# Performance work log

Hardware: AMD Instinct MI355X
Metric: run time of the kernel (lower is better)

## Reference

```python
import jax, jax.numpy as jnp
import numpy as np

C = 256      # channels (multiple of 32 for GroupNorm)
K = 3        # kernel
PAD = 1      # padding
G = 32       # GroupNorm groups
EPS = 1e-5


def setup_inputs() -> dict:
    key = jax.random.key(0)
    ks = jax.random.split(key, 7)
    B, H, W = 4, 64, 64
    return {
        "x": jax.random.normal(ks[0], (B, C, H, W), jnp.float32),
        "offset": jax.random.normal(ks[1], (B, 2 * K * K, H, W), jnp.float32),
        "weight": jax.random.normal(ks[2], (C, C, K, K), jnp.float32) * 0.01,
        "att_w": jax.random.normal(ks[3], (1, C), jnp.float32) * 0.01,
        "att_b": jnp.zeros((1,), jnp.float32),
        "gamma": jnp.ones((C,), jnp.float32),
        "beta": jnp.zeros((C,), jnp.float32),
    }


def _bilinear_one(xb, py, px):
    # xb: [C, H, W]; py, px: [KK, H, W] fractional sample coords (zero-pad outside)
    H, W = xb.shape[1], xb.shape[2]
    y0 = jnp.floor(py)
    x0 = jnp.floor(px)
    y1 = y0 + 1.0
    x1 = x0 + 1.0
    wy1 = py - y0
    wy0 = 1.0 - wy1
    wx1 = px - x0
    wx0 = 1.0 - wx1

    def g(yi, xi):
        valid = (yi >= 0) & (yi < H) & (xi >= 0) & (xi < W)
        yc = jnp.clip(yi, 0, H - 1).astype(jnp.int32)
        xc = jnp.clip(xi, 0, W - 1).astype(jnp.int32)
        return xb[:, yc, xc] * valid[None].astype(xb.dtype)  # [C, KK, H, W]

    return (g(y0, x0) * (wy0 * wx0)[None] + g(y0, x1) * (wy0 * wx1)[None]
            + g(y1, x0) * (wy1 * wx0)[None] + g(y1, x1) * (wy1 * wx1)[None])


def reference(x, offset, weight, att_w, att_b, gamma, beta):
    B, Cc, H, W = x.shape
    KK = K * K
    off = offset.reshape(B, KK, 2, H, W)  # (dy, dx) per kernel tap
    ii, jj = jnp.meshgrid(jnp.arange(K), jnp.arange(K), indexing='ij')
    dky = (ii - PAD).reshape(KK).astype(x.dtype)
    dkx = (jj - PAD).reshape(KK).astype(x.dtype)
    ys = jnp.arange(H, dtype=x.dtype)
    xs = jnp.arange(W, dtype=x.dtype)
    # sample coords [B, KK, H, W]
    py = ys[None, :, None] + dky[:, None, None] + off[:, :, 0]
    px = xs[None, None, :] + dkx[:, None, None] + off[:, :, 1]

    # deformable unfold: [B, C, KK, H, W]
    xu = jax.vmap(_bilinear_one)(x, py, px)

    # max over kernel taps -> channel attention gate
    xm = xu.max(axis=2)  # [B, C, H, W]
    att = jax.nn.sigmoid(jnp.einsum('bchw,oc->bohw', xm, att_w)
                         + att_b[None, :, None, None])  # [B, 1, H, W]

    # gate the unfolded samples, then emulate the conv as one GEMM
    xw = xu * att[:, :, None]  # broadcast over C, KK
    cols = xw.transpose(1, 2, 0, 3, 4).reshape(Cc * KK, B * H * W)  # [C*KK, BHW]
    out = (weight.reshape(Cc, Cc * KK) @ cols).reshape(Cc, B, H, W).transpose(1, 0, 2, 3)

    # GroupNorm(32, C) + ReLU
    og = out.reshape(B, G, Cc // G, H, W)
    mu = og.mean(axis=(2, 3, 4), keepdims=True)
    var = og.var(axis=(2, 3, 4), keepdims=True)
    on = ((og - mu) * jax.lax.rsqrt(var + EPS)).reshape(B, Cc, H, W)
    return jax.nn.relu(on * gamma[None, :, None, None] + beta[None, :, None, None])
```

## Files before the change

### kernel.cpp

```cpp
#include <hip/hip_runtime.h>

#define CT 256
#define KDIM 2304
#define COLP 296

typedef unsigned short u16;
typedef _Float16 h2 __attribute__((ext_vector_type(2)));
typedef _Float16 h8 __attribute__((ext_vector_type(8)));
typedef __attribute__((ext_vector_type(4))) float f32x4;

__device__ __forceinline__ unsigned pkh(float a, float b) {
    h2 r; r[0] = (_Float16)a; r[1] = (_Float16)b;
    return __builtin_bit_cast(unsigned, r);
}

__device__ __forceinline__ void gload_lds16(const uint4* g, u16* l) {
    __builtin_amdgcn_global_load_lds((const __attribute__((address_space(1))) void*)g,
                                     (__attribute__((address_space(3))) void*)l, 16, 0, 0);
}

__global__ __launch_bounds__(256) void k_prep(const float* __restrict__ x, uint4* __restrict__ xi,
                                              const float* __restrict__ wgt, uint4* __restrict__ pw)
{
    if (blockIdx.x < 2048) {
        int u = blockIdx.x * 256 + threadIdx.x;
        int bcg = u >> 12, p = u & 4095;
        const float* xp = x + (((size_t)bcg) << 15) + p;
        unsigned r[4];
#pragma unroll
        for (int i = 0; i < 4; ++i)
            r[i] = pkh(xp[(size_t)(2 * i) << 12], xp[(size_t)(2 * i + 1) << 12]);
        uint4 o; o.x = r[0]; o.y = r[1]; o.z = r[2]; o.w = r[3];
        xi[u] = o;
    } else {
        int u = (blockIdx.x - 2048) * 256 + threadIdx.x;
        int kc = u >> 10, rm = u & 1023;
        int m = rm >> 2, j = rm & 3;
        int round = kc / 9, tap = kc - round * 9;
        const float* src = wgt + (size_t)m * KDIM + tap;
        int c0 = round * 32 + j * 8;
        unsigned q[4];
#pragma unroll
        for (int i = 0; i < 4; ++i)
            q[i] = pkh(src[(size_t)(c0 + 2 * i) * 9], src[(size_t)(c0 + 2 * i + 1) * 9]);
        uint4 o; o.x = q[0]; o.y = q[1]; o.z = q[2]; o.w = q[3];
        pw[u] = o;
    }
}

__device__ __forceinline__ void gather_one(int it2, int sp, int xsb, size_t gfall,
                                           const uint2* s_wt, const int2* s_off,
                                           const u16* Xs, u16* col,
                                           const uint4* __restrict__ xi, int rbase, int nw)
{
    int tap = it2 >> 5, nn = it2 & 31;
    uint2 wp = s_wt[it2];
    h2 w01 = __builtin_bit_cast(h2, wp.x);
    h2 w23 = __builtin_bit_cast(h2, wp.y);
    h2 wxp = (h2){w01[0], w01[0]}, wyp = (h2){w01[1], w01[1]};
    h2 wzp = (h2){w23[0], w23[0]}, wwp = (h2){w23[1], w23[1]};
    int2 of = s_off[it2];
    int P00 = of.x & 0xffff, P01 = (of.x >> 16) & 0xffff;
    int P10 = of.y & 0xffff, P11 = (of.y >> 16) & 0xffff;
    uint4 c00, c01, c10, c11;
    int Q;
    Q = P00 - rbase;
    if ((unsigned)Q < (unsigned)nw) c00 = *(const uint4*)&Xs[xsb + Q * 8]; else c00 = xi[gfall + P00];
    Q = P01 - rbase;
    if ((unsigned)Q < (unsigned)nw) c01 = *(const uint4*)&Xs[xsb + Q * 8]; else c01 = xi[gfall + P01];
    Q = P10 - rbase;
    if ((unsigned)Q < (unsigned)nw) c10 = *(const uint4*)&Xs[xsb + Q * 8]; else c10 = xi[gfall + P10];
    Q = P11 - rbase;
    if ((unsigned)Q < (unsigned)nw) c11 = *(const uint4*)&Xs[xsb + Q * 8]; else c11 = xi[gfall + P11];
    const unsigned* a00 = (const unsigned*)&c00;
    const unsigned* a01 = (const unsigned*)&c01;
    const unsigned* a10 = (const unsigned*)&c10;
    const unsigned* a11 = (const unsigned*)&c11;
    unsigned o[4];
#pragma unroll
    for (int q = 0; q < 4; ++q) {
        h2 r = wxp * __builtin_bit_cast(h2, a00[q]) + wyp * __builtin_bit_cast(h2, a01[q])
             + wzp * __builtin_bit_cast(h2, a10[q]) + wwp * __builtin_bit_cast(h2, a11[q]);
        o[q] = __builtin_bit_cast(unsigned, r);
    }
    uint4 ov; ov.x = o[0]; ov.y = o[1]; ov.z = o[2]; ov.w = o[3];
    *(uint4*)&col[nn * COLP + tap * 32 + sp * 8] = ov;
}

__global__ __launch_bounds__(512, 2) void k_main(const uint4* __restrict__ xi, const float* __restrict__ off,
                                                 const uint4* __restrict__ pw, const float* __restrict__ att_w,
                                                 const float* __restrict__ att_b,
                                                 float* __restrict__ outp, float* __restrict__ gnpart)
{
    __shared__ uint2 s_wt[288];
    __shared__ int2 s_off[288];
    __shared__ u16 Xs[4 * 6656];
    __shared__ u16 col[32 * COLP];
    __shared__ float s_att[32];

    int rowblk = blockIdx.x >> 1, half = blockIdx.x & 1;
    int b = rowblk >> 6, h = rowblk & 63, n0 = half * 32;
    int tid = threadIdx.x;
    int lane = tid & 63, w = tid >> 6;
    int l15 = lane & 15, kb = lane >> 4;
    int wm = w * 32;
    int nn_a = w * 4 + (lane >> 4);
    int ca = (lane & 15) * 2;

    for (int e = tid; e < 288; e += 512) {
        int kk = e >> 5, wl = e & 31;
        int ww_ = n0 + wl;
        int ky = kk / 3, kx = kk - ky * 3;
        float dy = off[((size_t)(b * 18 + 2 * kk) * 64 + h) * 64 + ww_];
        float dx = off[((size_t)(b * 18 + 2 * kk + 1) * 64 + h) * 64 + ww_];
        float py = (float)(h + ky - 1) + dy;
        float px = (float)(ww_ + kx - 1) + dx;
        float y0f = floorf(py), x0f = floorf(px);
        int y0 = (int)y0f, x0 = (int)x0f;
        float fy = py - y0f, fx = px - x0f;
        float vy0 = (y0 >= 0 && y0 < 64) ? 1.f : 0.f;
        float vy1 = (y0 >= -1 && y0 < 63) ? 1.f : 0.f;
        float vx0 = (x0 >= 0 && x0 < 64) ? 1.f : 0.f;
        float vx1 = (x0 >= -1 && x0 < 63) ? 1.f : 0.f;
        float w0 = (1.f - fy) * (1.f - fx) * vy0 * vx0;
        float w1 = (1.f - fy) * fx * vy0 * vx1;
        float w2 = fy * (1.f - fx) * vy1 * vx0;
        float w3 = fy * fx * vy1 * vx1;
        uint2 wp;
        wp.x = pkh(w0, w1);
        wp.y = pkh(w2, w3);
        int yc0 = min(max(y0, 0), 63), yc1 = min(max(y0 + 1, 0), 63);
        int xc0 = min(max(x0, 0), 63), xc1 = min(max(x0 + 1, 0), 63);
        s_wt[e] = wp;
        s_off[e] = make_int2((yc0 * 64 + xc0) | ((yc0 * 64 + xc1) << 16),
                             (yc1 * 64 + xc0) | ((yc1 * 64 + xc1) << 16));
    }

    int r0 = max(0, h - 6), r1 = min(63, h + 6);
    int nrows = r1 - r0 + 1, nw = nrows * 64, rbase = r0 * 64;
    size_t xib = (size_t)(b * 32) << 12;

    float att_acc = 0.f;
    f32x4 acc[2][2];
#pragma unroll
    for (int mt = 0; mt < 2; ++mt)
#pragma unroll
        for (int nt = 0; nt < 2; ++nt) acc[mt][nt] = (f32x4){0.f, 0.f, 0.f, 0.f};

    int pwoff[2];
#pragma unroll
    for (int mt = 0; mt < 2; ++mt) pwoff[mt] = (wm + mt * 16 + l15) * 4 + kb;

#pragma unroll
    for (int cgl = 0; cgl < 2; ++cgl)
        for (int e = tid; e < nw; e += 512)
            gload_lds16(&xi[xib + ((size_t)cgl << 12) + rbase + e], &Xs[(cgl * 6656 + e * 8)]);

    for (int stage = 0; stage < 16; ++stage) {
        int buf = stage & 1;
        int s2 = stage & 1;
        __syncthreads();
        if (stage < 15) {
            size_t nb = xib + ((size_t)((stage + 1) * 2) << 12) + rbase;
#pragma unroll
            for (int cgl = 0; cgl < 2; ++cgl)
                for (int e = tid; e < nw; e += 512)
                    gload_lds16(&xi[nb + ((size_t)cgl << 12) + e],
                                &Xs[(((buf ^ 1) * 2 + cgl) * 6656 + e * 8)]);
        }
        {
            int it = tid;
            int cgl = (it >= 288) ? 1 : 0;
            gather_one(it - cgl * 288, s2 * 2 + cgl, (buf * 2 + cgl) * 6656,
                       xib + ((size_t)(stage * 2 + cgl) << 12), s_wt, s_off, Xs, col, xi, rbase, nw);
            if (tid >= 448) {
                int it2 = tid + 64;
                gather_one(it2 - 288, s2 * 2 + 1, (buf * 2 + 1) * 6656,
                           xib + ((size_t)(stage * 2 + 1) << 12), s_wt, s_off, Xs, col, xi, rbase, nw);
            }
        }

        if (stage & 1) {
            int round = stage >> 1;
            __syncthreads();

            uint4 aa[4][2];
#pragma unroll
            for (int ts = 0; ts < 4; ++ts)
#pragma unroll
                for (int mt = 0; mt < 2; ++mt)
                    aa[ts][mt] = pw[(size_t)(round * 9 + ts) * 1024 + pwoff[mt]];

            {
                int sp = ca >> 3, co = ca & 7;
                const u16* base = &col[nn_a * COLP + sp * 8 + co];
                float m0 = -1e30f, m1 = -1e30f;
#pragma unroll
                for (int t = 0; t < 9; ++t) {
                    unsigned v = *(const unsigned*)(base + t * 32);
                    h2 vv = __builtin_bit_cast(h2, v);
                    m0 = fmaxf(m0, (float)vv[0]);
                    m1 = fmaxf(m1, (float)vv[1]);
                }
                int cb = round * 32 + ca;
                att_acc += att_w[cb] * m0 + att_w[cb + 1] * m1;
            }

#pragma unroll
            for (int ts = 0; ts < 9; ++ts) {
                h8 bf[2];
#pragma unroll
                for (int nt = 0; nt < 2; ++nt)
                    bf[nt] = *(const h8*)&col[(nt * 16 + l15) * COLP + ts * 32 + kb * 8];
                h8 af[2];
#pragma unroll
                for (int mt = 0; mt < 2; ++mt) af[mt] = __builtin_bit_cast(h8, aa[ts & 3][mt]);
                if (ts + 4 < 9) {
#pragma unroll
                    for (int mt = 0; mt < 2; ++mt)
                        aa[ts & 3][mt] = pw[(size_t)(round * 9 + ts + 4) * 1024 + pwoff[mt]];
                }
#pragma unroll
                for (int mt = 0; mt < 2; ++mt)
#pragma unroll
                    for (int nt = 0; nt < 2; ++nt)
                        acc[mt][nt] = __builtin_amdgcn_mfma_f32_16x16x32_f16(af[mt], bf[nt], acc[mt][nt], 0, 0, 0);
            }
        }
    }

#pragma unroll
    for (int d = 1; d <= 8; d <<= 1) att_acc += __shfl_xor(att_acc, d);
    if ((lane & 15) == 0) s_att[nn_a] = 1.f / (1.f + expf(-(att_acc + att_b[0])));
    __syncthreads();

    float attn[2];
#pragma unroll
    for (int nt = 0; nt < 2; ++nt) attn[nt] = s_att[nt * 16 + l15];

#pragma unroll
    for (int mt = 0; mt < 2; ++mt) {
        float s1 = 0.f, s2 = 0.f;
#pragma unroll
        for (int nt = 0; nt < 2; ++nt)
#pragma unroll
            for (int r = 0; r < 4; ++r) {
                float v = acc[mt][nt][r] * attn[nt];
                int m = wm + mt * 16 + kb * 4 + r;
                outp[(((size_t)(b * CT + m)) << 12) + h * 64 + n0 + nt * 16 + l15] = v;
                s1 += v; s2 += v * v;
            }
#pragma unroll
        for (int d = 1; d <= 16; d <<= 1) {
            s1 += __shfl_xor(s1, d);
            s2 += __shfl_xor(s2, d);
        }
        if ((lane & 31) == 0) {
            int gidx = w * 4 + mt * 2 + (kb >> 1);
            gnpart[blockIdx.x * 64 + gidx * 2] = s1;
            gnpart[blockIdx.x * 64 + gidx * 2 + 1] = s2;
        }
    }
}

__global__ __launch_bounds__(256) void k_gn(const float* __restrict__ gnpart, const float* __restrict__ gamma,
                                            const float* __restrict__ beta, float* __restrict__ outp)
{
    __shared__ float rs1[128], rs2[128];
    __shared__ float s_stat[2];
    int bg = blockIdx.x;
    int b = bg >> 5, g = bg & 31;
    int tid = threadIdx.x;
    if (tid < 128) {
        int blk = (b * 64 + (tid >> 1)) * 2 + (tid & 1);
        rs1[tid] = gnpart[blk * 64 + g * 2];
        rs2[tid] = gnpart[blk * 64 + g * 2 + 1];
    }
    __syncthreads();
    if (tid < 64) {
        float a = rs1[tid] + rs1[tid + 64];
        float c = rs2[tid] + rs2[tid + 64];
#pragma unroll
        for (int d = 1; d <= 32; d <<= 1) {
            a += __shfl_xor(a, d);
            c += __shfl_xor(c, d);
        }
        if (tid == 0) {
            float mean = a * (1.f / 32768.f);
            float var = c * (1.f / 32768.f) - mean * mean;
            s_stat[0] = mean;
            s_stat[1] = rsqrtf(var + 1e-5f);
        }
    }
    __syncthreads();
    float mean = s_stat[0], rstd = s_stat[1];
    float4* p4 = (float4*)(outp + ((size_t)(b * CT + g * 8) << 12));
    for (int i = tid; i < 8192; i += 256) {
        int c = g * 8 + (i >> 10);
        float ga = gamma[c], be = beta[c];
        float4 v = p4[i];
        float4 r;
        r.x = fmaxf((v.x - mean) * rstd * ga + be, 0.f);
        r.y = fmaxf((v.y - mean) * rstd * ga + be, 0.f);
        r.z = fmaxf((v.z - mean) * rstd * ga + be, 0.f);
        r.w = fmaxf((v.w - mean) * rstd * ga + be, 0.f);
        p4[i] = r;
    }
}

extern "C" void kernel_launch(void* const* d_in, const int* in_sizes, int n_in,
                              void* d_out, int out_size, void* d_ws, size_t ws_size,
                              hipStream_t stream)
{
    const float* x = (const float*)d_in[0];
    const float* off = (const float*)d_in[1];
    const float* wgt = (const float*)d_in[2];
    const float* attw = (const float*)d_in[3];
    const float* attb = (const float*)d_in[4];
    const float* gamma = (const float*)d_in[5];
    const float* beta = (const float*)d_in[6];
    float* outp = (float*)d_out;

    char* ws = (char*)d_ws;
    uint4* xi = (uint4*)ws;
    uint4* pw = (uint4*)(ws + 8388608);
    float* gnpart = (float*)(ws + 9568256);

    k_prep<<<dim3(2336), dim3(256), 0, stream>>>(x, xi, wgt, pw);
    k_main<<<dim3(512), dim3(512), 0, stream>>>(xi, off, pw, attw, attb, outp, gnpart);
    k_gn<<<dim3(128), dim3(256), 0, stream>>>(gnpart, gamma, beta, outp);
}
```

Baseline: 147.1 us.

## Gather directly from global into double-buffered col, overlapping with MFMA

```diff
diff --git a/kernel.cpp b/kernel.cpp
--- a/kernel.cpp
+++ b/kernel.cpp
@@ -3,6 +3,7 @@
 #define CT 256
 #define KDIM 2304
 #define COLP 296
+#define CSZ (32 * COLP)
 
 typedef unsigned short u16;
 typedef _Float16 h2 __attribute__((ext_vector_type(2)));
@@ -12,11 +13,6 @@
 __device__ __forceinline__ unsigned pkh(float a, float b) {
     h2 r; r[0] = (_Float16)a; r[1] = (_Float16)b;
     return __builtin_bit_cast(unsigned, r);
-}
-
-__device__ __forceinline__ void gload_lds16(const uint4* g, u16* l) {
-    __builtin_amdgcn_global_load_lds((const __attribute__((address_space(1))) void*)g,
-                                     (__attribute__((address_space(3))) void*)l, 16, 0, 0);
 }
 
 __global__ __launch_bounds__(256) void k_prep(const float* __restrict__ x, uint4* __restrict__ xi,
@@ -48,54 +44,58 @@
     }
 }
 
-__device__ __forceinline__ void gather_one(int it2, int sp, int xsb, size_t gfall,
-                                           const uint2* s_wt, const int2* s_off,
-                                           const u16* Xs, u16* col,
-                                           const uint4* __restrict__ xi, int rbase, int nw)
-{
-    int tap = it2 >> 5, nn = it2 & 31;
-    uint2 wp = s_wt[it2];
-    h2 w01 = __builtin_bit_cast(h2, wp.x);
-    h2 w23 = __builtin_bit_cast(h2, wp.y);
+struct GB {
+    uint4 c00, c01, c10, c11;
+    unsigned wx, wy;
+    int dst;
+};
+
+__device__ __forceinline__ void g_load(int it, int round, size_t xib,
+                                       const uint2* s_wt, const int2* s_off,
+                                       const uint4* __restrict__ xi, GB& g)
+{
+    int sp = it / 288;
+    int rem = it - sp * 288;
+    uint2 wp = s_wt[rem];
+    int2 of = s_off[rem];
+    g.wx = wp.x; g.wy = wp.y;
+    const uint4* gp = xi + xib + ((size_t)((round << 2) + sp) << 12);
+    g.c00 = gp[of.x & 0xffff];
+    g.c01 = gp[(of.x >> 16) & 0xffff];
+    g.c10 = gp[of.y & 0xffff];
+    g.c11 = gp[(of.y >> 16) & 0xffff];
+    g.dst = (rem & 31) * COLP + (rem >> 5) * 32 + (sp << 3);
+}
+
+__device__ __forceinline__ void g_fin(const GB& g, u16* colb)
+{
+    h2 w01 = __builtin_bit_cast(h2, g.wx);
+    h2 w23 = __builtin_bit_cast(h2, g.wy);
     h2 wxp = (h2){w01[0], w01[0]}, wyp = (h2){w01[1], w01[1]};
     h2 wzp = (h2){w23[0], w23[0]}, wwp = (h2){w23[1], w23[1]};
-    int2 of = s_off[it2];
-    int P00 = of.x & 0xffff, P01 = (of.x >> 16) & 0xffff;
-    int P10 = of.y & 0xffff, P11 = (of.y >> 16) & 0xffff;
-    uint4 c00, c01, c10, c11;
-    int Q;
-    Q = P00 - rbase;
-    if ((unsigned)Q < (unsigned)nw) c00 = *(const uint4*)&Xs[xsb + Q * 8]; else c00 = xi[gfall + P00];
-    Q = P01 - rbase;
-    if ((unsigned)Q < (unsigned)nw) c01 = *(const uint4*)&Xs[xsb + Q * 8]; else c01 = xi[gfall + P01];
-    Q = P10 - rbase;
-    if ((unsigned)Q < (unsigned)nw) c10 = *(const uint4*)&Xs[xsb + Q * 8]; else c10 = xi[gfall + P10];
-    Q = P11 - rbase;
-    if ((unsigned)Q < (unsigned)nw) c11 = *(const uint4*)&Xs[xsb + Q * 8]; else c11 = xi[gfall + P11];
-    const unsigned* a00 = (const unsigned*)&c00;
-    const unsigned* a01 = (const unsigned*)&c01;
-    const unsigned* a10 = (const unsigned*)&c10;
-    const unsigned* a11 = (const unsigned*)&c11;
+    const unsigned* a00 = (const unsigned*)&g.c00;
+    const unsigned* a01 = (const unsigned*)&g.c01;
+    const unsigned* a10 = (const unsigned*)&g.c10;
+    const unsigned* a11 = (const unsigned*)&g.c11;
     unsigned o[4];
 #pragma unroll
     for (int q = 0; q < 4; ++q) {
-        h2 r = wxp * __builtin_bit_cast(h2, a00[q]) + wyp * __builtin_bit_cast(h2, a01[q])
-             + wzp * __builtin_bit_cast(h2, a10[q]) + wwp * __builtin_bit_cast(h2, a11[q]);
-        o[q] = __builtin_bit_cast(unsigned, r);
+        h2 rr = wxp * __builtin_bit_cast(h2, a00[q]) + wyp * __builtin_bit_cast(h2, a01[q])
+              + wzp * __builtin_bit_cast(h2, a10[q]) + wwp * __builtin_bit_cast(h2, a11[q]);
+        o[q] = __builtin_bit_cast(unsigned, rr);
     }
     uint4 ov; ov.x = o[0]; ov.y = o[1]; ov.z = o[2]; ov.w = o[3];
-    *(uint4*)&col[nn * COLP + tap * 32 + sp * 8] = ov;
-}
-
-__global__ __launch_bounds__(512, 2) void k_main(const uint4* __restrict__ xi, const float* __restrict__ off,
+    *(uint4*)&colb[g.dst] = ov;
+}
+
+__global__ __launch_bounds__(512, 4) void k_main(const uint4* __restrict__ xi, const float* __restrict__ off,
                                                  const uint4* __restrict__ pw, const float* __restrict__ att_w,
                                                  const float* __restrict__ att_b,
                                                  float* __restrict__ outp, float* __restrict__ gnpart)
 {
     __shared__ uint2 s_wt[288];
     __shared__ int2 s_off[288];
-    __shared__ u16 Xs[4 * 6656];
-    __shared__ u16 col[32 * COLP];
+    __shared__ u16 col[2 * CSZ];
     __shared__ float s_att[32];
 
     int rowblk = blockIdx.x >> 1, half = blockIdx.x & 1;
@@ -136,8 +136,6 @@
                              (yc1 * 64 + xc0) | ((yc1 * 64 + xc1) << 16));
     }
 
-    int r0 = max(0, h - 6), r1 = min(63, h + 6);
-    int nrows = r1 - r0 + 1, nw = nrows * 64, rbase = r0 * 64;
     size_t xib = (size_t)(b * 32) << 12;
 
     float att_acc = 0.f;
@@ -151,82 +149,87 @@
 #pragma unroll
     for (int mt = 0; mt < 2; ++mt) pwoff[mt] = (wm + mt * 16 + l15) * 4 + kb;
 
-#pragma unroll
-    for (int cgl = 0; cgl < 2; ++cgl)
-        for (int e = tid; e < nw; e += 512)
-            gload_lds16(&xi[xib + ((size_t)cgl << 12) + rbase + e], &Xs[(cgl * 6656 + e * 8)]);
-
-    for (int stage = 0; stage < 16; ++stage) {
-        int buf = stage & 1;
-        int s2 = stage & 1;
+    __syncthreads();
+
+    {
+        GB g0, g1;
+        g_load(tid, 0, xib, s_wt, s_off, xi, g0);
+        g_load(tid + 512, 0, xib, s_wt, s_off, xi, g1);
+        g_fin(g0, col);
+        g_fin(g1, col);
+        if (tid < 128) {
+            GB g2;
+            g_load(tid + 1024, 0, xib, s_wt, s_off, xi, g2);
+            g_fin(g2, col);
+        }
+    }
+
+    uint4 aa[4][2];
+#pragma unroll
+    for (int ts = 0; ts < 4; ++ts)
+#pragma unroll
+        for (int mt = 0; mt < 2; ++mt)
+            aa[ts][mt] = pw[(size_t)ts * 1024 + pwoff[mt]];
+
+    __syncthreads();
+
+    for (int r = 0; r < 8; ++r) {
+        u16* cb = col + (r & 1) * CSZ;
+        u16* nb = col + ((r & 1) ^ 1) * CSZ;
+
+        GB g0, g1, g2;
+        if (r < 7) g_load(tid, r + 1, xib, s_wt, s_off, xi, g0);
+
+        {
+            int spa = ca >> 3, co = ca & 7;
+            const u16* base = &cb[nn_a * COLP + spa * 8 + co];
+            float m0 = -1e30f, m1 = -1e30f;
+#pragma unroll
+            for (int t = 0; t < 9; ++t) {
+                unsigned v = *(const unsigned*)(base + t * 32);
+                h2 vv = __builtin_bit_cast(h2, v);
+                m0 = fmaxf(m0, (float)vv[0]);
+                m1 = fmaxf(m1, (float)vv[1]);
+            }
+            int cbx = r * 32 + ca;
+            att_acc += att_w[cbx] * m0 + att_w[cbx + 1] * m1;
+        }
+
+#pragma unroll
+        for (int ts = 0; ts < 9; ++ts) {
+            h8 bf[2];
+#pragma unroll
+            for (int nt = 0; nt < 2; ++nt)
+                bf[nt] = *(const h8*)&cb[(nt * 16 + l15) * COLP + ts * 32 + kb * 8];
+            h8 af[2];
+#pragma unroll
+            for (int mt = 0; mt < 2; ++mt) af[mt] = __builtin_bit_cast(h8, aa[ts & 3][mt]);
+            if (ts + 4 < 9) {
+#pragma unroll
+                for (int mt = 0; mt < 2; ++mt)
+                    aa[ts & 3][mt] = pw[(size_t)(r * 9 + ts + 4) * 1024 + pwoff[mt]];
+            } else if (r < 7) {
+                int tsp = (ts == 8) ? 0 : (ts - 4);
+#pragma unroll
+                for (int mt = 0; mt < 2; ++mt)
+                    aa[tsp][mt] = pw[(size_t)((r + 1) * 9 + tsp) * 1024 + pwoff[mt]];
+            }
+#pragma unroll
+            for (int mt = 0; mt < 2; ++mt)
+#pragma unroll
+                for (int nt = 0; nt < 2; ++nt)
+                    acc[mt][nt] = __builtin_amdgcn_mfma_f32_16x16x32_f16(af[mt], bf[nt], acc[mt][nt], 0, 0, 0);
+            if (ts == 2 && r < 7) {
+                g_fin(g0, nb);
+                g_load(tid + 512, r + 1, xib, s_wt, s_off, xi, g1);
+            }
+            if (ts == 5 && r < 7) {
+                g_fin(g1, nb);
+                if (tid < 128) g_load(tid + 1024, r + 1, xib, s_wt, s_off, xi, g2);
+            }
+        }
+        if (r < 7 && tid < 128) g_fin(g2, nb);
         __syncthreads();
-        if (stage < 15) {
-            size_t nb = xib + ((size_t)((stage + 1) * 2) << 12) + rbase;
-#pragma unroll
-            for (int cgl = 0; cgl < 2; ++cgl)
-                for (int e = tid; e < nw; e += 512)
-                    gload_lds16(&xi[nb + ((size_t)cgl << 12) + e],
-                                &Xs[(((buf ^ 1) * 2 + cgl) * 6656 + e * 8)]);
-        }
-        {
-            int it = tid;
-            int cgl = (it >= 288) ? 1 : 0;
-            gather_one(it - cgl * 288, s2 * 2 + cgl, (buf * 2 + cgl) * 6656,
-                       xib + ((size_t)(stage * 2 + cgl) << 12), s_wt, s_off, Xs, col, xi, rbase, nw);
-            if (tid >= 448) {
-                int it2 = tid + 64;
-                gather_one(it2 - 288, s2 * 2 + 1, (buf * 2 + 1) * 6656,
-                           xib + ((size_t)(stage * 2 + 1) << 12), s_wt, s_off, Xs, col, xi, rbase, nw);
-            }
-        }
-
-        if (stage & 1) {
-            int round = stage >> 1;
-            __syncthreads();
-
-            uint4 aa[4][2];
-#pragma unroll
-            for (int ts = 0; ts < 4; ++ts)
-#pragma unroll
-                for (int mt = 0; mt < 2; ++mt)
-                    aa[ts][mt] = pw[(size_t)(round * 9 + ts) * 1024 + pwoff[mt]];
-
-            {
-                int sp = ca >> 3, co = ca & 7;
-                const u16* base = &col[nn_a * COLP + sp * 8 + co];
-                float m0 = -1e30f, m1 = -1e30f;
-#pragma unroll
-                for (int t = 0; t < 9; ++t) {
-                    unsigned v = *(const unsigned*)(base + t * 32);
-                    h2 vv = __builtin_bit_cast(h2, v);
-                    m0 = fmaxf(m0, (float)vv[0]);
-                    m1 = fmaxf(m1, (float)vv[1]);
-                }
-                int cb = round * 32 + ca;
-                att_acc += att_w[cb] * m0 + att_w[cb + 1] * m1;
-            }
-
-#pragma unroll
-            for (int ts = 0; ts < 9; ++ts) {
-                h8 bf[2];
-#pragma unroll
-                for (int nt = 0; nt < 2; ++nt)
-                    bf[nt] = *(const h8*)&col[(nt * 16 + l15) * COLP + ts * 32 + kb * 8];
-                h8 af[2];
-#pragma unroll
-                for (int mt = 0; mt < 2; ++mt) af[mt] = __builtin_bit_cast(h8, aa[ts & 3][mt]);
-                if (ts + 4 < 9) {
-#pragma unroll
-                    for (int mt = 0; mt < 2; ++mt)
-                        aa[ts & 3][mt] = pw[(size_t)(round * 9 + ts + 4) * 1024 + pwoff[mt]];
-                }
-#pragma unroll
-                for (int mt = 0; mt < 2; ++mt)
-#pragma unroll
-                    for (int nt = 0; nt < 2; ++nt)
-                        acc[mt][nt] = __builtin_amdgcn_mfma_f32_16x16x32_f16(af[mt], bf[nt], acc[mt][nt], 0, 0, 0);
-            }
-        }
     }
 
 #pragma unroll
```

After: 168.7 us. 14.7% more time.

## Double-buffer im2col tile to overlap gather with MFMA, remap blocks per XCD

Applied to the files above, without the earlier changes.

```diff
diff --git a/kernel.cpp b/kernel.cpp
--- a/kernel.cpp
+++ b/kernel.cpp
@@ -3,6 +3,8 @@
 #define CT 256
 #define KDIM 2304
 #define COLP 296
+#define CCOL (32 * COLP)
+#define XSP 4608
 
 typedef unsigned short u16;
 typedef _Float16 h2 __attribute__((ext_vector_type(2)));
@@ -94,12 +96,18 @@
 {
     __shared__ uint2 s_wt[288];
     __shared__ int2 s_off[288];
-    __shared__ u16 Xs[4 * 6656];
-    __shared__ u16 col[32 * COLP];
+    __shared__ u16 Xs[4 * XSP];
+    __shared__ u16 col[2 * CCOL];
     __shared__ float s_att[32];
 
-    int rowblk = blockIdx.x >> 1, half = blockIdx.x & 1;
-    int b = rowblk >> 6, h = rowblk & 63, n0 = half * 32;
+    int bid = blockIdx.x;
+    int xcd = bid & 7, idx = bid >> 3;
+    int b = xcd >> 1;
+    int local = ((xcd & 1) << 6) + idx;
+    int h = local >> 1, half = local & 1;
+    int lbid = b * 128 + local;
+    int n0 = half * 32;
+
     int tid = threadIdx.x;
     int lane = tid & 63, w = tid >> 6;
     int l15 = lane & 15, kb = lane >> 4;
@@ -136,8 +144,8 @@
                              (yc1 * 64 + xc0) | ((yc1 * 64 + xc1) << 16));
     }
 
-    int r0 = max(0, h - 6), r1 = min(63, h + 6);
-    int nrows = r1 - r0 + 1, nw = nrows * 64, rbase = r0 * 64;
+    int r0c = max(0, h - 4), r1c = min(63, h + 4);
+    int nrows = r1c - r0c + 1, nw = nrows * 64, rbase = r0c * 64;
     size_t xib = (size_t)(b * 32) << 12;
 
     float att_acc = 0.f;
@@ -154,11 +162,10 @@
 #pragma unroll
     for (int cgl = 0; cgl < 2; ++cgl)
         for (int e = tid; e < nw; e += 512)
-            gload_lds16(&xi[xib + ((size_t)cgl << 12) + rbase + e], &Xs[(cgl * 6656 + e * 8)]);
+            gload_lds16(&xi[xib + ((size_t)cgl << 12) + rbase + e], &Xs[(cgl * XSP + e * 8)]);
 
     for (int stage = 0; stage < 16; ++stage) {
         int buf = stage & 1;
-        int s2 = stage & 1;
         __syncthreads();
         if (stage < 15) {
             size_t nb = xib + ((size_t)((stage + 1) * 2) << 12) + rbase;
@@ -166,34 +173,23 @@
             for (int cgl = 0; cgl < 2; ++cgl)
                 for (int e = tid; e < nw; e += 512)
                     gload_lds16(&xi[nb + ((size_t)cgl << 12) + e],
-                                &Xs[(((buf ^ 1) * 2 + cgl) * 6656 + e * 8)]);
-        }
-        {
-            int it = tid;
-            int cgl = (it >= 288) ? 1 : 0;
-            gather_one(it - cgl * 288, s2 * 2 + cgl, (buf * 2 + cgl) * 6656,
-                       xib + ((size_t)(stage * 2 + cgl) << 12), s_wt, s_off, Xs, col, xi, rbase, nw);
-            if (tid >= 448) {
-                int it2 = tid + 64;
-                gather_one(it2 - 288, s2 * 2 + 1, (buf * 2 + 1) * 6656,
-                           xib + ((size_t)(stage * 2 + 1) << 12), s_wt, s_off, Xs, col, xi, rbase, nw);
-            }
-        }
-
-        if (stage & 1) {
-            int round = stage >> 1;
-            __syncthreads();
+                                &Xs[(((buf ^ 1) * 2 + cgl) * XSP + e * 8)]);
+        }
+
+        if (stage >= 2 && !(stage & 1)) {
+            int rr = (stage >> 1) - 1;
+            const u16* cb = col + (rr & 1) * CCOL;
 
             uint4 aa[4][2];
 #pragma unroll
             for (int ts = 0; ts < 4; ++ts)
 #pragma unroll
                 for (int mt = 0; mt < 2; ++mt)
-                    aa[ts][mt] = pw[(size_t)(round * 9 + ts) * 1024 + pwoff[mt]];
+                    aa[ts][mt] = pw[(size_t)(rr * 9 + ts) * 1024 + pwoff[mt]];
 
             {
                 int sp = ca >> 3, co = ca & 7;
-                const u16* base = &col[nn_a * COLP + sp * 8 + co];
+                const u16* base = &cb[nn_a * COLP + sp * 8 + co];
                 float m0 = -1e30f, m1 = -1e30f;
 #pragma unroll
                 for (int t = 0; t < 9; ++t) {
@@ -202,8 +198,8 @@
                     m0 = fmaxf(m0, (float)vv[0]);
                     m1 = fmaxf(m1, (float)vv[1]);
                 }
-                int cb = round * 32 + ca;
-                att_acc += att_w[cb] * m0 + att_w[cb + 1] * m1;
+                int cbx = rr * 32 + ca;
+                att_acc += att_w[cbx] * m0 + att_w[cbx + 1] * m1;
             }
 
 #pragma unroll
@@ -211,14 +207,14 @@
                 h8 bf[2];
 #pragma unroll
                 for (int nt = 0; nt < 2; ++nt)
-                    bf[nt] = *(const h8*)&col[(nt * 16 + l15) * COLP + ts * 32 + kb * 8];
+                    bf[nt] = *(const h8*)&cb[(nt * 16 + l15) * COLP + ts * 32 + kb * 8];
                 h8 af[2];
 #pragma unroll
                 for (int mt = 0; mt < 2; ++mt) af[mt] = __builtin_bit_cast(h8, aa[ts & 3][mt]);
                 if (ts + 4 < 9) {
 #pragma unroll
                     for (int mt = 0; mt < 2; ++mt)
-                        aa[ts & 3][mt] = pw[(size_t)(round * 9 + ts + 4) * 1024 + pwoff[mt]];
+                        aa[ts & 3][mt] = pw[(size_t)(rr * 9 + ts + 4) * 1024 + pwoff[mt]];
                 }
 #pragma unroll
                 for (int mt = 0; mt < 2; ++mt)
@@ -226,6 +222,65 @@
                     for (int nt = 0; nt < 2; ++nt)
                         acc[mt][nt] = __builtin_amdgcn_mfma_f32_16x16x32_f16(af[mt], bf[nt], acc[mt][nt], 0, 0, 0);
             }
+        }
+
+        {
+            u16* cw = col + ((stage >> 1) & 1) * CCOL;
+            int it = tid;
+            int cgl = (it >= 288) ? 1 : 0;
+            gather_one(it - cgl * 288, buf * 2 + cgl, (buf * 2 + cgl) * XSP,
+                       xib + ((size_t)(stage * 2 + cgl) << 12), s_wt, s_off, Xs, cw, xi, rbase, nw);
+            if (tid >= 448) {
+                int it2 = tid + 64;
+                gather_one(it2 - 288, buf * 2 + 1, (buf * 2 + 1) * XSP,
+                           xib + ((size_t)(stage * 2 + 1) << 12), s_wt, s_off, Xs, cw, xi, rbase, nw);
+            }
+        }
+    }
+
+    __syncthreads();
+    {
+        int rr = 7;
+        const u16* cb = col + (rr & 1) * CCOL;
+        uint4 aa[4][2];
+#pragma unroll
+        for (int ts = 0; ts < 4; ++ts)
+#pragma unroll
+            for (int mt = 0; mt < 2; ++mt)
+                aa[ts][mt] = pw[(size_t)(rr * 9 + ts) * 1024 + pwoff[mt]];
+        {
+            int sp = ca >> 3, co = ca & 7;
+            const u16* base = &cb[nn_a * COLP + sp * 8 + co];
+            float m0 = -1e30f, m1 = -1e30f;
+#pragma unroll
+            for (int t = 0; t < 9; ++t) {
+                unsigned v = *(const unsigned*)(base + t * 32);
+                h2 vv = __builtin_bit_cast(h2, v);
+                m0 = fmaxf(m0, (float)vv[0]);
+                m1 = fmaxf(m1, (float)vv[1]);
+            }
+            int cbx = rr * 32 + ca;
+            att_acc += att_w[cbx] * m0 + att_w[cbx + 1] * m1;
+        }
+#pragma unroll
+        for (int ts = 0; ts < 9; ++ts) {
+            h8 bf[2];
+#pragma unroll
+            for (int nt = 0; nt < 2; ++nt)
+                bf[nt] = *(const h8*)&cb[(nt * 16 + l15) * COLP + ts * 32 + kb * 8];
+            h8 af[2];
+#pragma unroll
+            for (int mt = 0; mt < 2; ++mt) af[mt] = __builtin_bit_cast(h8, aa[ts & 3][mt]);
+            if (ts + 4 < 9) {
+#pragma unroll
+                for (int mt = 0; mt < 2; ++mt)
+                    aa[ts & 3][mt] = pw[(size_t)(rr * 9 + ts + 4) * 1024 + pwoff[mt]];
+            }
+#pragma unroll
+            for (int mt = 0; mt < 2; ++mt)
+#pragma unroll
+                for (int nt = 0; nt < 2; ++nt)
+                    acc[mt][nt] = __builtin_amdgcn_mfma_f32_16x16x32_f16(af[mt], bf[nt], acc[mt][nt], 0, 0, 0);
         }
     }
 
@@ -257,8 +312,8 @@
         }
         if ((lane & 31) == 0) {
             int gidx = w * 4 + mt * 2 + (kb >> 1);
-            gnpart[blockIdx.x * 64 + gidx * 2] = s1;
-            gnpart[blockIdx.x * 64 + gidx * 2 + 1] = s2;
+            gnpart[lbid * 64 + gidx * 2] = s1;
+            gnpart[lbid * 64 + gidx * 2 + 1] = s2;
         }
     }
 }
```

Measured after the change: 146.0 us, median of 2. No clear change (-0.7%).

## Split main kernel into 16-pixel tiles with XCD-aware mapping and smaller LDS

Applied to the files above, without the earlier changes.

```diff
diff --git a/kernel.cpp b/kernel.cpp
--- a/kernel.cpp
+++ b/kernel.cpp
@@ -3,6 +3,8 @@
 #define CT 256
 #define KDIM 2304
 #define COLP 296
+#define CCOLH (16 * COLP)
+#define XSP6 6656
 
 typedef unsigned short u16;
 typedef _Float16 h2 __attribute__((ext_vector_type(2)));
@@ -53,7 +55,7 @@
                                            const u16* Xs, u16* col,
                                            const uint4* __restrict__ xi, int rbase, int nw)
 {
-    int tap = it2 >> 5, nn = it2 & 31;
+    int tap = it2 >> 4, nn = it2 & 15;
     uint2 wp = s_wt[it2];
     h2 w01 = __builtin_bit_cast(h2, wp.x);
     h2 w23 = __builtin_bit_cast(h2, wp.y);
@@ -87,28 +89,35 @@
     *(uint4*)&col[nn * COLP + tap * 32 + sp * 8] = ov;
 }
 
-__global__ __launch_bounds__(512, 2) void k_main(const uint4* __restrict__ xi, const float* __restrict__ off,
+__global__ __launch_bounds__(512, 6) void k_main(const uint4* __restrict__ xi, const float* __restrict__ off,
                                                  const uint4* __restrict__ pw, const float* __restrict__ att_w,
                                                  const float* __restrict__ att_b,
                                                  float* __restrict__ outp, float* __restrict__ gnpart)
 {
-    __shared__ uint2 s_wt[288];
-    __shared__ int2 s_off[288];
-    __shared__ u16 Xs[4 * 6656];
-    __shared__ u16 col[32 * COLP];
-    __shared__ float s_att[32];
-
-    int rowblk = blockIdx.x >> 1, half = blockIdx.x & 1;
-    int b = rowblk >> 6, h = rowblk & 63, n0 = half * 32;
+    __shared__ uint2 s_wt[144];
+    __shared__ int2 s_off[144];
+    __shared__ __align__(16) u16 Xs[2 * XSP6];
+    __shared__ __align__(16) u16 col[2 * CCOLH];
+    __shared__ float s_att[16];
+
+    int bid = blockIdx.x;
+    int xcd = bid & 7, idx = bid >> 3;
+    int b = xcd >> 1;
+    int local = ((xcd & 1) << 7) + idx;
+    int h = local >> 2, q = local & 3;
+    int lbid = b * 256 + local;
+    int n0 = q * 16;
+
     int tid = threadIdx.x;
     int lane = tid & 63, w = tid >> 6;
     int l15 = lane & 15, kb = lane >> 4;
     int wm = w * 32;
-    int nn_a = w * 4 + (lane >> 4);
-    int ca = (lane & 15) * 2;
-
-    for (int e = tid; e < 288; e += 512) {
-        int kk = e >> 5, wl = e & 31;
+    int pos_a = w * 2 + (lane >> 5);
+    int sub = lane & 31;
+
+    if (tid < 144) {
+        int e = tid;
+        int kk = e >> 4, wl = e & 15;
         int ww_ = n0 + wl;
         int ky = kk / 3, kx = kk - ky * 3;
         float dy = off[((size_t)(b * 18 + 2 * kk) * 64 + h) * 64 + ww_];
@@ -136,16 +145,14 @@
                              (yc1 * 64 + xc0) | ((yc1 * 64 + xc1) << 16));
     }
 
-    int r0 = max(0, h - 6), r1 = min(63, h + 6);
-    int nrows = r1 - r0 + 1, nw = nrows * 64, rbase = r0 * 64;
+    int r0c = max(0, h - 6), r1c = min(63, h + 6);
+    int nrows = r1c - r0c + 1, nw = nrows * 64, rbase = r0c * 64;
     size_t xib = (size_t)(b * 32) << 12;
 
     float att_acc = 0.f;
-    f32x4 acc[2][2];
-#pragma unroll
-    for (int mt = 0; mt < 2; ++mt)
-#pragma unroll
-        for (int nt = 0; nt < 2; ++nt) acc[mt][nt] = (f32x4){0.f, 0.f, 0.f, 0.f};
+    f32x4 acc[2];
+#pragma unroll
+    for (int mt = 0; mt < 2; ++mt) acc[mt] = (f32x4){0.f, 0.f, 0.f, 0.f};
 
     int pwoff[2];
 #pragma unroll
@@ -154,102 +161,82 @@
 #pragma unroll
     for (int cgl = 0; cgl < 2; ++cgl)
         for (int e = tid; e < nw; e += 512)
-            gload_lds16(&xi[xib + ((size_t)cgl << 12) + rbase + e], &Xs[(cgl * 6656 + e * 8)]);
-
-    for (int stage = 0; stage < 16; ++stage) {
-        int buf = stage & 1;
-        int s2 = stage & 1;
+            gload_lds16(&xi[xib + ((size_t)cgl << 12) + rbase + e], &Xs[(cgl * XSP6 + e * 8)]);
+
+    for (int s = 0; s < 16; ++s) {
         __syncthreads();
-        if (stage < 15) {
-            size_t nb = xib + ((size_t)((stage + 1) * 2) << 12) + rbase;
+        if (tid < 288) {
+            u16* cw = col + ((s >> 1) & 1) * CCOLH;
+            int cgl = (tid >= 144) ? 1 : 0;
+            gather_one(tid - cgl * 144, (s & 1) * 2 + cgl, cgl * XSP6,
+                       xib + ((size_t)(s * 2 + cgl) << 12), s_wt, s_off, Xs, cw, xi, rbase, nw);
+        }
+        __syncthreads();
+        if (s < 15) {
+            size_t nb = xib + ((size_t)((s + 1) * 2) << 12) + rbase;
 #pragma unroll
             for (int cgl = 0; cgl < 2; ++cgl)
                 for (int e = tid; e < nw; e += 512)
-                    gload_lds16(&xi[nb + ((size_t)cgl << 12) + e],
-                                &Xs[(((buf ^ 1) * 2 + cgl) * 6656 + e * 8)]);
-        }
-        {
-            int it = tid;
-            int cgl = (it >= 288) ? 1 : 0;
-            gather_one(it - cgl * 288, s2 * 2 + cgl, (buf * 2 + cgl) * 6656,
-                       xib + ((size_t)(stage * 2 + cgl) << 12), s_wt, s_off, Xs, col, xi, rbase, nw);
-            if (tid >= 448) {
-                int it2 = tid + 64;
-                gather_one(it2 - 288, s2 * 2 + 1, (buf * 2 + 1) * 6656,
-                           xib + ((size_t)(stage * 2 + 1) << 12), s_wt, s_off, Xs, col, xi, rbase, nw);
+                    gload_lds16(&xi[nb + ((size_t)cgl << 12) + e], &Xs[(cgl * XSP6 + e * 8)]);
+        }
+
+        if (s & 1) {
+            int rr = s >> 1;
+            const u16* cb = col + (rr & 1) * CCOLH;
+
+            uint4 aa[4][2];
+#pragma unroll
+            for (int ts = 0; ts < 4; ++ts)
+#pragma unroll
+                for (int mt = 0; mt < 2; ++mt)
+                    aa[ts][mt] = pw[(size_t)(rr * 9 + ts) * 1024 + pwoff[mt]];
+
+            {
+                const u16* base = &cb[pos_a * COLP + (sub >> 3) * 8 + (sub & 7)];
+                float m0 = -1e30f;
+#pragma unroll
+                for (int t = 0; t < 9; ++t) {
+                    u16 v = base[t * 32];
+                    m0 = fmaxf(m0, (float)__builtin_bit_cast(_Float16, v));
+                }
+                att_acc += att_w[rr * 32 + sub] * m0;
             }
-        }
-
-        if (stage & 1) {
-            int round = stage >> 1;
-            __syncthreads();
-
-            uint4 aa[4][2];
-#pragma unroll
-            for (int ts = 0; ts < 4; ++ts)
-#pragma unroll
-                for (int mt = 0; mt < 2; ++mt)
-                    aa[ts][mt] = pw[(size_t)(round * 9 + ts) * 1024 + pwoff[mt]];
-
-            {
-                int sp = ca >> 3, co = ca & 7;
-                const u16* base = &col[nn_a * COLP + sp * 8 + co];
-                float m0 = -1e30f, m1 = -1e30f;
-#pragma unroll
-                for (int t = 0; t < 9; ++t) {
-                    unsigned v = *(const unsigned*)(base + t * 32);
-                    h2 vv = __builtin_bit_cast(h2, v);
-                    m0 = fmaxf(m0, (float)vv[0]);
-                    m1 = fmaxf(m1, (float)vv[1]);
-                }
-                int cb = round * 32 + ca;
-                att_acc += att_w[cb] * m0 + att_w[cb + 1] * m1;
-            }
 
 #pragma unroll
             for (int ts = 0; ts < 9; ++ts) {
-                h8 bf[2];
-#pragma unroll
-                for (int nt = 0; nt < 2; ++nt)
-                    bf[nt] = *(const h8*)&col[(nt * 16 + l15) * COLP + ts * 32 + kb * 8];
+                h8 bf = *(const h8*)&cb[l15 * COLP + ts * 32 + kb * 8];
                 h8 af[2];
 #pragma unroll
                 for (int mt = 0; mt < 2; ++mt) af[mt] = __builtin_bit_cast(h8, aa[ts & 3][mt]);
                 if (ts + 4 < 9) {
 #pragma unroll
                     for (int mt = 0; mt < 2; ++mt)
-                        aa[ts & 3][mt] = pw[(size_t)(round * 9 + ts + 4) * 1024 + pwoff[mt]];
+                        aa[ts & 3][mt] = pw[(size_t)(rr * 9 + ts + 4) * 1024 + pwoff[mt]];
                 }
 #pragma unroll
                 for (int mt = 0; mt < 2; ++mt)
-#pragma unroll
-                    for (int nt = 0; nt < 2; ++nt)
-                        acc[mt][nt] = __builtin_amdgcn_mfma_f32_16x16x32_f16(af[mt], bf[nt], acc[mt][nt], 0, 0, 0);
+                    acc[mt] = __builtin_amdgcn_mfma_f32_16x16x32_f16(af[mt], bf, acc[mt], 0, 0, 0);
             }
         }
     }
 
 #pragma unroll
-    for (int d = 1; d <= 8; d <<= 1) att_acc += __shfl_xor(att_acc, d);
-    if ((lane & 15) == 0) s_att[nn_a] = 1.f / (1.f + expf(-(att_acc + att_b[0])));
+    for (int d = 1; d <= 16; d <<= 1) att_acc += __shfl_xor(att_acc, d);
+    if ((lane & 31) == 0) s_att[pos_a] = 1.f / (1.f + expf(-(att_acc + att_b[0])));
     __syncthreads();
 
-    float attn[2];
-#pragma unroll
-    for (int nt = 0; nt < 2; ++nt) attn[nt] = s_att[nt * 16 + l15];
+    float attn = s_att[l15];
 
 #pragma unroll
     for (int mt = 0; mt < 2; ++mt) {
         float s1 = 0.f, s2 = 0.f;
 #pragma unroll
-        for (int nt = 0; nt < 2; ++nt)
-#pragma unroll
-            for (int r = 0; r < 4; ++r) {
-                float v = acc[mt][nt][r] * attn[nt];
-                int m = wm + mt * 16 + kb * 4 + r;
-                outp[(((size_t)(b * CT + m)) << 12) + h * 64 + n0 + nt * 16 + l15] = v;
-                s1 += v; s2 += v * v;
-            }
+        for (int r = 0; r < 4; ++r) {
+            float v = acc[mt][r] * attn;
+            int m = wm + mt * 16 + kb * 4 + r;
+            outp[(((size_t)(b * CT + m)) << 12) + h * 64 + n0 + l15] = v;
+            s1 += v; s2 += v * v;
+        }
 #pragma unroll
         for (int d = 1; d <= 16; d <<= 1) {
             s1 += __shfl_xor(s1, d);
@@ -257,8 +244,8 @@
         }
         if ((lane & 31) == 0) {
             int gidx = w * 4 + mt * 2 + (kb >> 1);
-            gnpart[blockIdx.x * 64 + gidx * 2] = s1;
-            gnpart[blockIdx.x * 64 + gidx * 2 + 1] = s2;
+            gnpart[(size_t)lbid * 64 + gidx * 2] = s1;
+            gnpart[(size_t)lbid * 64 + gidx * 2 + 1] = s2;
         }
     }
 }
@@ -266,38 +253,34 @@
 __global__ __launch_bounds__(256) void k_gn(const float* __restrict__ gnpart, const float* __restrict__ gamma,
                                             const float* __restrict__ beta, float* __restrict__ outp)
 {
-    __shared__ float rs1[128], rs2[128];
+    __shared__ float red1[4], red2[4];
     __shared__ float s_stat[2];
     int bg = blockIdx.x;
     int b = bg >> 5, g = bg & 31;
     int tid = threadIdx.x;
-    if (tid < 128) {
-        int blk = (b * 64 + (tid >> 1)) * 2 + (tid & 1);
-        rs1[tid] = gnpart[blk * 64 + g * 2];
-        rs2[tid] = gnpart[blk * 64 + g * 2 + 1];
-    }
+    float a = gnpart[(size_t)(b * 256 + tid) * 64 + g * 2];
+    float c = gnpart[(size_t)(b * 256 + tid) * 64 + g * 2 + 1];
+#pragma unroll
+    for (int d = 1; d <= 32; d <<= 1) {
+        a += __shfl_xor(a, d);
+        c += __shfl_xor(c, d);
+    }
+    if ((tid & 63) == 0) { red1[tid >> 6] = a; red2[tid >> 6] = c; }
     __syncthreads();
-    if (tid < 64) {
-        float a = rs1[tid] + rs1[tid + 64];
-        float c = rs2[tid] + rs2[tid + 64];
-#pragma unroll
-        for (int d = 1; d <= 32; d <<= 1) {
-            a += __shfl_xor(a, d);
-            c += __shfl_xor(c, d);
-        }
-        if (tid == 0) {
-            float mean = a * (1.f / 32768.f);
-            float var = c * (1.f / 32768.f) - mean * mean;
-            s_stat[0] = mean;
-            s_stat[1] = rsqrtf(var + 1e-5f);
-        }
+    if (tid == 0) {
+        float A = red1[0] + red1[1] + red1[2] + red1[3];
+        float C = red2[0] + red2[1] + red2[2] + red2[3];
+        float mean = A * (1.f / 32768.f);
+        float var = C * (1.f / 32768.f) - mean * mean;
+        s_stat[0] = mean;
+        s_stat[1] = rsqrtf(var + 1e-5f);
     }
     __syncthreads();
     float mean = s_stat[0], rstd = s_stat[1];
     float4* p4 = (float4*)(outp + ((size_t)(b * CT + g * 8) << 12));
     for (int i = tid; i < 8192; i += 256) {
-        int c = g * 8 + (i >> 10);
-        float ga = gamma[c], be = beta[c];
+        int c2 = g * 8 + (i >> 10);
+        float ga = gamma[c2], be = beta[c2];
         float4 v = p4[i];
         float4 r;
         r.x = fmaxf((v.x - mean) * rstd * ga + be, 0.f);
@@ -327,6 +310,6 @@
     float* gnpart = (float*)(ws + 9568256);
 
     k_prep<<<dim3(2336), dim3(256), 0, stream>>>(x, xi, wgt, pw);
-    k_main<<<dim3(512), dim3(512), 0, stream>>>(xi, off, pw, attw, attb, outp, gnpart);
+    k_main<<<dim3(1024), dim3(512), 0, stream>>>(xi, off, pw, attw, attb, outp, gnpart);
     k_gn<<<dim3(128), dim3(256), 0, stream>>>(gnpart, gamma, beta, outp);
 }
```

After: 180.8 us. 22.9% more time.
